# Performance work log

Measured on AMD Instinct MI355X. Metric: run time of the kernel, lower is better.

## Reference

```python
import jax, jax.numpy as jnp
import numpy as np

N_NODES = 100000
HIDDEN = 128
N_EDGES = 1600000


def setup_inputs() -> dict:
    key = jax.random.key(0)
    k_x, k_w, k_r, k_c = jax.random.split(key, 4)
    x = jax.random.normal(k_x, (4, N_NODES, HIDDEN), dtype=jnp.float32)
    W = jax.random.normal(k_w, (HIDDEN, HIDDEN), dtype=jnp.float32) * 0.05
    b = jnp.zeros((HIDDEN,), dtype=jnp.float32)
    # COO edge list of the block-diagonal adjacency (scipy.sparse.block_diag in original)
    rows = jax.random.randint(k_r, (N_EDGES,), 0, N_NODES, dtype=jnp.int64)
    cols = jax.random.randint(k_c, (N_EDGES,), 0, N_NODES, dtype=jnp.int64)
    return {"x": x, "W": W, "b": b, "rows": rows, "cols": cols}


def reference(x, W, b, rows, cols):
    n_nodes = x.shape[1]
    beta = x[3, :, 0]   # [N]
    gamma = x[3, :, 1]  # [N]
    # linear + sigmoid on S/I/R channels: [3, N, H]
    sir = jax.nn.sigmoid(jnp.einsum('snh,oh->sno', x[:3], W) + b)
    S, I = sir[0], sir[1]
    # AI[r] += I[c] for each edge (r, c) of block-diagonal adjacency
    AI = jax.ops.segment_sum(I[cols], rows, num_segments=n_nodes)
    dS = -beta[:, None] * AI * S
    dI = -dS - gamma[:, None] * I
    dR = gamma[:, None] * I
    return jnp.stack((dS, dI, dR, jnp.zeros_like(dS)))
```

## Files before the change

### kernel.cpp

```cpp
#include <hip/hip_runtime.h>
#include <math.h>

#define HD 128
#define BM 128

typedef short bf16x8 __attribute__((ext_vector_type(8)));
typedef float f32x4 __attribute__((ext_vector_type(4)));
typedef unsigned short u16;

static __device__ __forceinline__ u16 f2bf(float f) {
  unsigned int u = __float_as_uint(f);
  u += 0x7FFF + ((u >> 16) & 1);
  return (u16)(u >> 16);
}
static __device__ __forceinline__ float bf2f(u16 s) {
  return __uint_as_float(((unsigned int)s) << 16);
}

__global__ void __launch_bounds__(256) zero_kernel(float4* __restrict__ p, long n4) {
  long i = (long)blockIdx.x * blockDim.x + threadIdx.x;
  long stride = (long)gridDim.x * blockDim.x;
  float4 z = make_float4(0.f, 0.f, 0.f, 0.f);
  for (; i < n4; i += stride) p[i] = z;
}

__global__ void __launch_bounds__(512, 4) gemm_hist(
    const float* __restrict__ x, const float* __restrict__ W,
    const float* __restrict__ b, float* __restrict__ SI, int nrows,
    const int* __restrict__ rows, int* __restrict__ counts, int n_edges,
    int gblocks) {
  __shared__ u16 Wh[HD * HD];
  __shared__ u16 Wl[HD * HD];

  int tid = threadIdx.x;
  if (blockIdx.x >= gblocks) {
    int i = (blockIdx.x - gblocks) * 512 + tid;
    int stride = (gridDim.x - gblocks) * 512;
    for (; i < n_edges; i += stride) atomicAdd(&counts[rows[i]], 1);
    return;
  }

  for (int idx = tid; idx < HD * (HD / 8); idx += 512) {
    int r = idx >> 4;
    int c = idx & 15;
    const float4* src = (const float4*)(W + r * HD + c * 8);
    float4 a0 = src[0], a1 = src[1];
    float f[8] = {a0.x, a0.y, a0.z, a0.w, a1.x, a1.y, a1.z, a1.w};
    union { u16 s[8]; uint4 v; } Ph, Pl;
#pragma unroll
    for (int i = 0; i < 8; ++i) {
      u16 h = f2bf(f[i]);
      Ph.s[i] = h;
      Pl.s[i] = f2bf(f[i] - bf2f(h));
    }
    int dst = r * HD + ((c ^ (r & 15)) << 3);
    *(uint4*)&Wh[dst] = Ph.v;
    *(uint4*)&Wl[dst] = Pl.v;
  }
  __syncthreads();

  int w = tid >> 6;
  int l = tid & 63;
  int lr = l & 15;
  int lk = l >> 4;
  int rbase = blockIdx.x * BM + w * 16;
  int arow = rbase + lr;
  bool rowok = arow < nrows;

  bf16x8 ah[4], al[4];
#pragma unroll
  for (int s = 0; s < 4; ++s) {
    float f[8] = {0.f, 0.f, 0.f, 0.f, 0.f, 0.f, 0.f, 0.f};
    if (rowok) {
      const float4* src = (const float4*)(x + (long)arow * HD + (s * 4 + lk) * 8);
      float4 a0 = src[0], a1 = src[1];
      f[0] = a0.x; f[1] = a0.y; f[2] = a0.z; f[3] = a0.w;
      f[4] = a1.x; f[5] = a1.y; f[6] = a1.z; f[7] = a1.w;
    }
    union { u16 s16[8]; bf16x8 v; } Ph, Pl;
#pragma unroll
    for (int i = 0; i < 8; ++i) {
      u16 h = f2bf(f[i]);
      Ph.s16[i] = h;
      Pl.s16[i] = f2bf(f[i] - bf2f(h));
    }
    ah[s] = Ph.v;
    al[s] = Pl.v;
  }

#pragma unroll
  for (int ct = 0; ct < 8; ++ct) {
    int col = ct * 16 + lr;
    f32x4 acc = {0.f, 0.f, 0.f, 0.f};
#pragma unroll
    for (int s = 0; s < 4; ++s) {
      int cb = ((s * 4 + lk) ^ lr) << 3;
      bf16x8 bh = *(const bf16x8*)&Wh[col * HD + cb];
      bf16x8 bl = *(const bf16x8*)&Wl[col * HD + cb];
      acc = __builtin_amdgcn_mfma_f32_16x16x32_bf16(ah[s], bh, acc, 0, 0, 0);
      acc = __builtin_amdgcn_mfma_f32_16x16x32_bf16(al[s], bh, acc, 0, 0, 0);
      acc = __builtin_amdgcn_mfma_f32_16x16x32_bf16(ah[s], bl, acc, 0, 0, 0);
    }
    float bb = b[col];
#pragma unroll
    for (int j = 0; j < 4; ++j) {
      int grow = rbase + lk * 4 + j;
      if (grow < nrows) {
        float v = acc[j] + bb;
        SI[(long)grow * HD + col] = 1.f / (1.f + __expf(-v));
      }
    }
  }
}

#define SCAN_E 2048
__global__ void __launch_bounds__(256) scan_block(const int* __restrict__ cnt,
                                                  int* __restrict__ off,
                                                  int* __restrict__ bsum, int n) {
  __shared__ int tsum[256];
  int tid = threadIdx.x;
  int base = blockIdx.x * SCAN_E + tid * 8;
  int vals[8];
  int s = 0;
#pragma unroll
  for (int k = 0; k < 8; ++k) {
    int idx = base + k;
    vals[k] = (idx < n) ? cnt[idx] : 0;
    s += vals[k];
  }
  tsum[tid] = s;
  __syncthreads();
  for (int o = 1; o < 256; o <<= 1) {
    int add = (tid >= o) ? tsum[tid - o] : 0;
    __syncthreads();
    tsum[tid] += add;
    __syncthreads();
  }
  int tbase = tsum[tid] - s;
  int run = 0;
#pragma unroll
  for (int k = 0; k < 8; ++k) {
    int idx = base + k;
    if (idx < n) off[idx] = tbase + run;
    run += vals[k];
  }
  if (tid == 255) bsum[blockIdx.x] = tsum[255];
}

__global__ void __launch_bounds__(256) scan_top(int* __restrict__ bsum, int nb) {
  __shared__ int sh[256];
  int tid = threadIdx.x;
  if (nb <= 256) {
    int v = (tid < nb) ? bsum[tid] : 0;
    sh[tid] = v;
    __syncthreads();
    for (int o = 1; o < 256; o <<= 1) {
      int add = (tid >= o) ? sh[tid - o] : 0;
      __syncthreads();
      sh[tid] += add;
      __syncthreads();
    }
    if (tid < nb) bsum[tid] = sh[tid] - v;
  } else if (tid == 0) {
    int acc = 0;
    for (int i = 0; i < nb; ++i) { int v = bsum[i]; bsum[i] = acc; acc += v; }
  }
}

__global__ void __launch_bounds__(256) scan_add(int* __restrict__ off,
                                                const int* __restrict__ bsum,
                                                int n, int n_edges) {
  int base = blockIdx.x * SCAN_E + threadIdx.x * 8;
  int add = bsum[blockIdx.x];
#pragma unroll
  for (int k = 0; k < 8; ++k) {
    int idx = base + k;
    if (idx < n) off[idx] += add;
  }
  if (blockIdx.x == 0 && threadIdx.x == 0) off[n] = n_edges;
}

__global__ void __launch_bounds__(256) fill_csr(const int* __restrict__ rows,
                                                const int* __restrict__ cols,
                                                const int* __restrict__ off,
                                                int* __restrict__ cursor,
                                                int* __restrict__ ecol, int n_edges) {
  int i = blockIdx.x * 256 + threadIdx.x;
  int stride = gridDim.x * 256;
  for (; i < n_edges; i += stride) {
    int r = rows[i];
    int p = atomicAdd(&cursor[r], 1);
    ecol[off[r] + p] = cols[i];
  }
}

__global__ void __launch_bounds__(256) gather_finalize(const float* __restrict__ S,
                                                       const float* __restrict__ I,
                                                       const float* __restrict__ x3,
                                                       const int* __restrict__ off,
                                                       const int* __restrict__ ecol,
                                                       float* __restrict__ out,
                                                       int n_nodes) {
  int node = blockIdx.x * 4 + (threadIdx.x >> 6);
  if (node >= n_nodes) return;
  int lane = threadIdx.x & 63;

  int beg = off[node], end = off[node + 1];
  float2 acc = make_float2(0.f, 0.f);
  for (int j0 = beg; j0 < end; j0 += 64) {
    int myc = (j0 + lane < end) ? ecol[j0 + lane] : 0;
    int cnt = min(64, end - j0);
    int j = 0;
    for (; j + 3 < cnt; j += 4) {
      int c0 = __shfl(myc, j);
      int c1 = __shfl(myc, j + 1);
      int c2 = __shfl(myc, j + 2);
      int c3 = __shfl(myc, j + 3);
      float2 v0 = ((const float2*)(I + (long)c0 * HD))[lane];
      float2 v1 = ((const float2*)(I + (long)c1 * HD))[lane];
      float2 v2 = ((const float2*)(I + (long)c2 * HD))[lane];
      float2 v3 = ((const float2*)(I + (long)c3 * HD))[lane];
      acc.x += (v0.x + v1.x) + (v2.x + v3.x);
      acc.y += (v0.y + v1.y) + (v2.y + v3.y);
    }
    for (; j < cnt; ++j) {
      int c0 = __shfl(myc, j);
      float2 v0 = ((const float2*)(I + (long)c0 * HD))[lane];
      acc.x += v0.x;
      acc.y += v0.y;
    }
  }

  float beta  = x3[(long)node * HD + 0];
  float gamma = x3[(long)node * HD + 1];
  float2 s  = ((const float2*)(S + (long)node * HD))[lane];
  float2 ii = ((const float2*)(I + (long)node * HD))[lane];

  float2 dS, dI, dR;
  dS.x = -beta * acc.x * s.x;
  dS.y = -beta * acc.y * s.y;
  dI.x = -dS.x - gamma * ii.x;
  dI.y = -dS.y - gamma * ii.y;
  dR.x = gamma * ii.x;
  dR.y = gamma * ii.y;

  long p = (long)node * (HD / 2) + lane;
  long plane = (long)n_nodes * (HD / 2);
  float2* o = (float2*)out;
  o[p] = dS;
  o[plane + p] = dI;
  o[2 * plane + p] = dR;
  o[3 * plane + p] = make_float2(0.f, 0.f);
}

extern "C" void kernel_launch(void* const* d_in, const int* in_sizes, int n_in,
                              void* d_out, int out_size, void* d_ws, size_t ws_size,
                              hipStream_t stream) {
  const float* x = (const float*)d_in[0];
  const float* W = (const float*)d_in[1];
  const float* b = (const float*)d_in[2];
  const int* rows = (const int*)d_in[3];
  const int* cols = (const int*)d_in[4];
  float* out = (float*)d_out;

  int n_nodes = in_sizes[0] / (4 * HD);
  int n_edges = in_sizes[3];
  int nrows = 2 * n_nodes;

  float* S = (float*)d_ws;
  float* I = S + (long)n_nodes * HD;
  int* ib = (int*)(I + (long)n_nodes * HD);
  int npad = (n_nodes + 11) & ~3;
  int* counts  = ib;
  int* cursor  = counts + npad;
  int* offsets = cursor + npad;
  int* bsum    = offsets + npad;
  int* ecol    = bsum + 256;

  zero_kernel<<<(2 * npad / 4 + 255) / 256, 256, 0, stream>>>(
      (float4*)counts, 2 * npad / 4);

  int gblocks = (nrows + BM - 1) / BM;
  int hblocks = 256;
  gemm_hist<<<gblocks + hblocks, 512, 0, stream>>>(x, W, b, S, nrows,
                                                   rows, counts, n_edges, gblocks);

  int nb = (n_nodes + SCAN_E - 1) / SCAN_E;
  scan_block<<<nb, 256, 0, stream>>>(counts, offsets, bsum, n_nodes);
  scan_top<<<1, 256, 0, stream>>>(bsum, nb);
  scan_add<<<nb, 256, 0, stream>>>(offsets, bsum, n_nodes, n_edges);

  int eb = min(2048, (n_edges + 255) / 256);
  fill_csr<<<eb, 256, 0, stream>>>(rows, cols, offsets, cursor, ecol, n_edges);

  int gfb = (n_nodes + 3) / 4;
  gather_finalize<<<gfb, 256, 0, stream>>>(S, I, x + 3 * (long)n_nodes * HD,
                                           offsets, ecol, out, n_nodes);
}
```

Before: 621.4 us.

## Overlap CSR fill with GEMM instead of histogram, fold scan_top into scan_add

The histogram pass becomes its own small kernel. The CSR fill, which is more expensive and atomic-heavy, is now co-scheduled inside the GEMM launch, so fill blocks run alongside the sigmoid-linear blocks and the scatter latency is hidden behind MFMA work. The separate scan_top launch is removed: each scan_add block serially sums the preceding block totals itself, which saves a launch at the cost of a small redundant serial loop. A risk is that fill blocks at the low block indices occupy CUs while the GEMM tail waits, and the standalone histogram no longer overlaps with anything.

```diff
diff --git a/kernel.cpp b/kernel.cpp
--- a/kernel.cpp
+++ b/kernel.cpp
@@ -24,93 +24,11 @@
   for (; i < n4; i += stride) p[i] = z;
 }
 
-__global__ void __launch_bounds__(512, 4) gemm_hist(
-    const float* __restrict__ x, const float* __restrict__ W,
-    const float* __restrict__ b, float* __restrict__ SI, int nrows,
-    const int* __restrict__ rows, int* __restrict__ counts, int n_edges,
-    int gblocks) {
-  __shared__ u16 Wh[HD * HD];
-  __shared__ u16 Wl[HD * HD];
-
-  int tid = threadIdx.x;
-  if (blockIdx.x >= gblocks) {
-    int i = (blockIdx.x - gblocks) * 512 + tid;
-    int stride = (gridDim.x - gblocks) * 512;
-    for (; i < n_edges; i += stride) atomicAdd(&counts[rows[i]], 1);
-    return;
-  }
-
-  for (int idx = tid; idx < HD * (HD / 8); idx += 512) {
-    int r = idx >> 4;
-    int c = idx & 15;
-    const float4* src = (const float4*)(W + r * HD + c * 8);
-    float4 a0 = src[0], a1 = src[1];
-    float f[8] = {a0.x, a0.y, a0.z, a0.w, a1.x, a1.y, a1.z, a1.w};
-    union { u16 s[8]; uint4 v; } Ph, Pl;
-#pragma unroll
-    for (int i = 0; i < 8; ++i) {
-      u16 h = f2bf(f[i]);
-      Ph.s[i] = h;
-      Pl.s[i] = f2bf(f[i] - bf2f(h));
-    }
-    int dst = r * HD + ((c ^ (r & 15)) << 3);
-    *(uint4*)&Wh[dst] = Ph.v;
-    *(uint4*)&Wl[dst] = Pl.v;
-  }
-  __syncthreads();
-
-  int w = tid >> 6;
-  int l = tid & 63;
-  int lr = l & 15;
-  int lk = l >> 4;
-  int rbase = blockIdx.x * BM + w * 16;
-  int arow = rbase + lr;
-  bool rowok = arow < nrows;
-
-  bf16x8 ah[4], al[4];
-#pragma unroll
-  for (int s = 0; s < 4; ++s) {
-    float f[8] = {0.f, 0.f, 0.f, 0.f, 0.f, 0.f, 0.f, 0.f};
-    if (rowok) {
-      const float4* src = (const float4*)(x + (long)arow * HD + (s * 4 + lk) * 8);
-      float4 a0 = src[0], a1 = src[1];
-      f[0] = a0.x; f[1] = a0.y; f[2] = a0.z; f[3] = a0.w;
-      f[4] = a1.x; f[5] = a1.y; f[6] = a1.z; f[7] = a1.w;
-    }
-    union { u16 s16[8]; bf16x8 v; } Ph, Pl;
-#pragma unroll
-    for (int i = 0; i < 8; ++i) {
-      u16 h = f2bf(f[i]);
-      Ph.s16[i] = h;
-      Pl.s16[i] = f2bf(f[i] - bf2f(h));
-    }
-    ah[s] = Ph.v;
-    al[s] = Pl.v;
-  }
-
-#pragma unroll
-  for (int ct = 0; ct < 8; ++ct) {
-    int col = ct * 16 + lr;
-    f32x4 acc = {0.f, 0.f, 0.f, 0.f};
-#pragma unroll
-    for (int s = 0; s < 4; ++s) {
-      int cb = ((s * 4 + lk) ^ lr) << 3;
-      bf16x8 bh = *(const bf16x8*)&Wh[col * HD + cb];
-      bf16x8 bl = *(const bf16x8*)&Wl[col * HD + cb];
-      acc = __builtin_amdgcn_mfma_f32_16x16x32_bf16(ah[s], bh, acc, 0, 0, 0);
-      acc = __builtin_amdgcn_mfma_f32_16x16x32_bf16(al[s], bh, acc, 0, 0, 0);
-      acc = __builtin_amdgcn_mfma_f32_16x16x32_bf16(ah[s], bl, acc, 0, 0, 0);
-    }
-    float bb = b[col];
-#pragma unroll
-    for (int j = 0; j < 4; ++j) {
-      int grow = rbase + lk * 4 + j;
-      if (grow < nrows) {
-        float v = acc[j] + bb;
-        SI[(long)grow * HD + col] = 1.f / (1.f + __expf(-v));
-      }
-    }
-  }
+__global__ void __launch_bounds__(256) hist_rows(const int* __restrict__ rows,
+                                                 int* __restrict__ cnt, int n_edges) {
+  int i = blockIdx.x * 256 + threadIdx.x;
+  int stride = gridDim.x * 256;
+  for (; i < n_edges; i += stride) atomicAdd(&cnt[rows[i]], 1);
 }
 
 #define SCAN_E 2048
@@ -147,31 +65,18 @@
   if (tid == 255) bsum[blockIdx.x] = tsum[255];
 }
 
-__global__ void __launch_bounds__(256) scan_top(int* __restrict__ bsum, int nb) {
-  __shared__ int sh[256];
-  int tid = threadIdx.x;
-  if (nb <= 256) {
-    int v = (tid < nb) ? bsum[tid] : 0;
-    sh[tid] = v;
-    __syncthreads();
-    for (int o = 1; o < 256; o <<= 1) {
-      int add = (tid >= o) ? sh[tid - o] : 0;
-      __syncthreads();
-      sh[tid] += add;
-      __syncthreads();
-    }
-    if (tid < nb) bsum[tid] = sh[tid] - v;
-  } else if (tid == 0) {
-    int acc = 0;
-    for (int i = 0; i < nb; ++i) { int v = bsum[i]; bsum[i] = acc; acc += v; }
-  }
-}
-
 __global__ void __launch_bounds__(256) scan_add(int* __restrict__ off,
                                                 const int* __restrict__ bsum,
-                                                int n, int n_edges) {
+                                                int nb, int n, int n_edges) {
+  __shared__ int sAdd;
+  if (threadIdx.x == 0) {
+    int acc = 0;
+    for (int i = 0; i < (int)blockIdx.x; ++i) acc += bsum[i];
+    sAdd = acc;
+  }
+  __syncthreads();
+  int add = sAdd;
   int base = blockIdx.x * SCAN_E + threadIdx.x * 8;
-  int add = bsum[blockIdx.x];
 #pragma unroll
   for (int k = 0; k < 8; ++k) {
     int idx = base + k;
@@ -180,17 +85,97 @@
   if (blockIdx.x == 0 && threadIdx.x == 0) off[n] = n_edges;
 }
 
-__global__ void __launch_bounds__(256) fill_csr(const int* __restrict__ rows,
-                                                const int* __restrict__ cols,
-                                                const int* __restrict__ off,
-                                                int* __restrict__ cursor,
-                                                int* __restrict__ ecol, int n_edges) {
-  int i = blockIdx.x * 256 + threadIdx.x;
-  int stride = gridDim.x * 256;
-  for (; i < n_edges; i += stride) {
-    int r = rows[i];
-    int p = atomicAdd(&cursor[r], 1);
-    ecol[off[r] + p] = cols[i];
+__global__ void __launch_bounds__(512, 4) fill_gemm(
+    const float* __restrict__ x, const float* __restrict__ W,
+    const float* __restrict__ b, float* __restrict__ SI, int nrows,
+    const int* __restrict__ rows, const int* __restrict__ cols,
+    const int* __restrict__ off, int* __restrict__ cursor,
+    int* __restrict__ ecol, int n_edges, int fblocks) {
+  __shared__ u16 Wh[HD * HD];
+  __shared__ u16 Wl[HD * HD];
+
+  int tid = threadIdx.x;
+  if (blockIdx.x < fblocks) {
+    int i = blockIdx.x * 512 + tid;
+    int stride = fblocks * 512;
+    for (; i < n_edges; i += stride) {
+      int r = rows[i];
+      int p = atomicAdd(&cursor[r], 1);
+      ecol[off[r] + p] = cols[i];
+    }
+    return;
+  }
+
+  for (int idx = tid; idx < HD * (HD / 8); idx += 512) {
+    int r = idx >> 4;
+    int c = idx & 15;
+    const float4* src = (const float4*)(W + r * HD + c * 8);
+    float4 a0 = src[0], a1 = src[1];
+    float f[8] = {a0.x, a0.y, a0.z, a0.w, a1.x, a1.y, a1.z, a1.w};
+    union { u16 s[8]; uint4 v; } Ph, Pl;
+#pragma unroll
+    for (int i = 0; i < 8; ++i) {
+      u16 h = f2bf(f[i]);
+      Ph.s[i] = h;
+      Pl.s[i] = f2bf(f[i] - bf2f(h));
+    }
+    int dst = r * HD + ((c ^ (r & 15)) << 3);
+    *(uint4*)&Wh[dst] = Ph.v;
+    *(uint4*)&Wl[dst] = Pl.v;
+  }
+  __syncthreads();
+
+  int w = tid >> 6;
+  int l = tid & 63;
+  int lr = l & 15;
+  int lk = l >> 4;
+  int rbase = (blockIdx.x - fblocks) * BM + w * 16;
+  int arow = rbase + lr;
+  bool rowok = arow < nrows;
+
+  bf16x8 ah[4], al[4];
+#pragma unroll
+  for (int s = 0; s < 4; ++s) {
+    float f[8] = {0.f, 0.f, 0.f, 0.f, 0.f, 0.f, 0.f, 0.f};
+    if (rowok) {
+      const float4* src = (const float4*)(x + (long)arow * HD + (s * 4 + lk) * 8);
+      float4 a0 = src[0], a1 = src[1];
+      f[0] = a0.x; f[1] = a0.y; f[2] = a0.z; f[3] = a0.w;
+      f[4] = a1.x; f[5] = a1.y; f[6] = a1.z; f[7] = a1.w;
+    }
+    union { u16 s16[8]; bf16x8 v; } Ph, Pl;
+#pragma unroll
+    for (int i = 0; i < 8; ++i) {
+      u16 h = f2bf(f[i]);
+      Ph.s16[i] = h;
+      Pl.s16[i] = f2bf(f[i] - bf2f(h));
+    }
+    ah[s] = Ph.v;
+    al[s] = Pl.v;
+  }
+
+#pragma unroll
+  for (int ct = 0; ct < 8; ++ct) {
+    int col = ct * 16 + lr;
+    f32x4 acc = {0.f, 0.f, 0.f, 0.f};
+#pragma unroll
+    for (int s = 0; s < 4; ++s) {
+      int cb = ((s * 4 + lk) ^ lr) << 3;
+      bf16x8 bh = *(const bf16x8*)&Wh[col * HD + cb];
+      bf16x8 bl = *(const bf16x8*)&Wl[col * HD + cb];
+      acc = __builtin_amdgcn_mfma_f32_16x16x32_bf16(ah[s], bh, acc, 0, 0, 0);
+      acc = __builtin_amdgcn_mfma_f32_16x16x32_bf16(al[s], bh, acc, 0, 0, 0);
+      acc = __builtin_amdgcn_mfma_f32_16x16x32_bf16(ah[s], bl, acc, 0, 0, 0);
+    }
+    float bb = b[col];
+#pragma unroll
+    for (int j = 0; j < 4; ++j) {
+      int grow = rbase + lk * 4 + j;
+      if (grow < nrows) {
+        float v = acc[j] + bb;
+        SI[(long)grow * HD + col] = 1.f / (1.f + __expf(-v));
+      }
+    }
   }
 }
 
@@ -280,18 +265,16 @@
   zero_kernel<<<(2 * npad / 4 + 255) / 256, 256, 0, stream>>>(
       (float4*)counts, 2 * npad / 4);
 
-  int gblocks = (nrows + BM - 1) / BM;
-  int hblocks = 256;
-  gemm_hist<<<gblocks + hblocks, 512, 0, stream>>>(x, W, b, S, nrows,
-                                                   rows, counts, n_edges, gblocks);
+  hist_rows<<<512, 256, 0, stream>>>(rows, counts, n_edges);
 
   int nb = (n_nodes + SCAN_E - 1) / SCAN_E;
   scan_block<<<nb, 256, 0, stream>>>(counts, offsets, bsum, n_nodes);
-  scan_top<<<1, 256, 0, stream>>>(bsum, nb);
-  scan_add<<<nb, 256, 0, stream>>>(offsets, bsum, n_nodes, n_edges);
-
-  int eb = min(2048, (n_edges + 255) / 256);
-  fill_csr<<<eb, 256, 0, stream>>>(rows, cols, offsets, cursor, ecol, n_edges);
+  scan_add<<<nb, 256, 0, stream>>>(offsets, bsum, nb, n_nodes, n_edges);
+
+  int gblocks = (nrows + BM - 1) / BM;
+  int fblocks = 192;
+  fill_gemm<<<fblocks + gblocks, 512, 0, stream>>>(
+      x, W, b, S, nrows, rows, cols, offsets, cursor, ecol, n_edges, fblocks);
 
   int gfb = (n_nodes + 3) / 4;
   gather_finalize<<<gfb, 256, 0, stream>>>(S, I, x + 3 * (long)n_nodes * HD,
```

Result: faster. 602.4 us (-3.1%).
